# Kernel tuning notes

Hardware: AMD Instinct MI355X
Metric: run time of the kernel (lower is better)

The kernel has to match this reference:

```python
import jax, jax.numpy as jnp
import numpy as np

IN_F = 256
OUT_F = 256
HYPER = 128
BATCH = 4096


def setup_inputs() -> dict:
    key = jax.random.key(0)
    ks = jax.random.split(key, 9)
    s_in = 1.0 / np.sqrt(IN_F)
    s_h = 1.0 / np.sqrt(HYPER)
    x = jax.random.normal(ks[0], (BATCH, IN_F), dtype=jnp.float32)
    # weight_gen: Linear(in, hyper) -> ReLU -> Linear(hyper, in*out)
    W1g = jax.random.uniform(ks[1], (IN_F, HYPER), jnp.float32, -s_in, s_in)
    b1g = jax.random.uniform(ks[2], (HYPER,), jnp.float32, -s_in, s_in)
    W2g = jax.random.uniform(ks[3], (HYPER, IN_F * OUT_F), jnp.float32, -s_h, s_h)
    b2g = jax.random.uniform(ks[4], (IN_F * OUT_F,), jnp.float32, -s_h, s_h)
    # bias_gen: Linear(in, hyper) -> ReLU -> Linear(hyper, out)
    W1b = jax.random.uniform(ks[5], (IN_F, HYPER), jnp.float32, -s_in, s_in)
    b1b = jax.random.uniform(ks[6], (HYPER,), jnp.float32, -s_in, s_in)
    W2b = jax.random.uniform(ks[7], (HYPER, OUT_F), jnp.float32, -s_h, s_h)
    b2b = jax.random.uniform(ks[8], (OUT_F,), jnp.float32, -s_h, s_h)
    return {"x": x, "W1g": W1g, "b1g": b1g, "W2g": W2g, "b2g": b2g,
            "W1b": W1b, "b1b": b1b, "W2b": W2b, "b2b": b2b}


def reference(x, W1g, b1g, W2g, b2g, W1b, b1b, W2b, b2b):
    B = x.shape[0]
    # generate per-sample weights [B, out, in]
    hg = jax.nn.relu(x @ W1g + b1g)                      # [B, hyper]
    weights = (hg @ W2g + b2g).reshape(B, OUT_F, IN_F)   # [B, out, in]
    # generate per-sample bias [B, out]
    hb = jax.nn.relu(x @ W1b + b1b)                      # [B, hyper]
    bias = hb @ W2b + b2b                                # [B, out]
    # batched matvec: bmm(weights, x[...,None]) + bias
    out = jnp.einsum('boi,bi->bo', weights, x) + bias    # [B, out]
    return out
```

## Files before the change

kernel.cpp:

```cpp
#include <hip/hip_runtime.h>

#define AS1 __attribute__((address_space(1)))
#define AS3 __attribute__((address_space(3)))

typedef short short8 __attribute__((ext_vector_type(8)));
typedef float f32x16 __attribute__((ext_vector_type(16)));
typedef unsigned short ushort4v __attribute__((ext_vector_type(4)));

#define BATCH 4096
#define IN_F 256
#define OUT_F 256
#define HYP 128
#define HX 129
#define KP (HX * IN_F)
#define NGEMMP 32
#define NVB 516

__device__ __forceinline__ float bf2f(unsigned short u) {
  unsigned v = ((unsigned)u) << 16;
  float f;
  __builtin_memcpy(&f, &v, 4);
  return f;
}
__device__ __forceinline__ unsigned short f2bf(float f) {
  unsigned u;
  __builtin_memcpy(&u, &f, 4);
  unsigned r = u + 0x7fffu + ((u >> 16) & 1u);
  return (unsigned short)(r >> 16);
}

__device__ __forceinline__ void gld_lds16(const unsigned short* g, unsigned short* s) {
  __builtin_amdgcn_global_load_lds((const AS1 unsigned int*)g, (AS3 unsigned int*)s, 16, 0, 0);
}

__global__ __launch_bounds__(256) void k_trans(const float* __restrict__ W1g,
                                               const float* __restrict__ W1b,
                                               const float* __restrict__ W2b,
                                               unsigned short* __restrict__ W1T,
                                               unsigned short* __restrict__ W2bT) {
  const int t = threadIdx.x, b = blockIdx.x;
  if (b < 64) {
#pragma unroll
    for (int i = 0; i < 4; ++i) {
      const int e = b * 1024 + i * 256 + t;
      const int n = e >> 8, k = e & 255;
      const float v = (n < HYP) ? W1g[k * HYP + n] : W1b[k * HYP + (n - HYP)];
      W1T[e] = f2bf(v);
    }
  } else {
#pragma unroll
    for (int i = 0; i < 4; ++i) {
      const int e = (b - 64) * 1024 + i * 256 + t;
      const int o = e >> 7, h = e & 127;
      W2bT[e] = f2bf(W2b[h * OUT_F + o]);
    }
  }
}

__global__ __launch_bounds__(512) void k_prep(
    const float* __restrict__ x,
    const float* __restrict__ b1g, const float* __restrict__ b1b,
    const float* __restrict__ b2b,
    const float* __restrict__ W2g, const float* __restrict__ b2g,
    const unsigned short* __restrict__ W1T, const unsigned short* __restrict__ W2bT,
    unsigned short* __restrict__ Vb, unsigned short* __restrict__ hgbT,
    unsigned short* __restrict__ xb, float* __restrict__ out) {
  __shared__ __align__(16) unsigned short xS[128 * 256];
  __shared__ __align__(16) unsigned short hbS[128 * 128];
  const int t = threadIdx.x;

  if (blockIdx.x >= NGEMMP) {
    const int base = (blockIdx.x - NGEMMP) * 2048 + t;
#pragma unroll
    for (int it = 0; it < 4; ++it) {
      const int cid = base + it * 512;
      const int ic = cid & 31;
      const int pair = cid >> 5;
      const int h = pair % HX;
      const int o = pair / HX;
      const float* src = (h < HYP) ? (W2g + (size_t)h * (OUT_F * IN_F) + o * IN_F + ic * 8)
                                   : (b2g + o * IN_F + ic * 8);
      const float4 v0 = ((const float4*)src)[0];
      const float4 v1 = ((const float4*)src)[1];
      uint4 pk;
      pk.x = (unsigned)f2bf(v0.x) | ((unsigned)f2bf(v0.y) << 16);
      pk.y = (unsigned)f2bf(v0.z) | ((unsigned)f2bf(v0.w) << 16);
      pk.z = (unsigned)f2bf(v1.x) | ((unsigned)f2bf(v1.y) << 16);
      pk.w = (unsigned)f2bf(v1.z) | ((unsigned)f2bf(v1.w) << 16);
      *(uint4*)(Vb + (size_t)o * KP + h * IN_F + ic * 8) = pk;
    }
    return;
  }

  const int lane = t & 63;
  const int w = t >> 6;
  const int l31 = lane & 31;
  const int hi = lane >> 5;
  const int m0 = blockIdx.x * 128;

#pragma unroll
  for (int j = 0; j < 16; ++j) {
    const int row = j * 8 + w;
    const float4 v = *(const float4*)(x + (size_t)(m0 + row) * IN_F + lane * 4);
    uint2 pk;
    pk.x = (unsigned)f2bf(v.x) | ((unsigned)f2bf(v.y) << 16);
    pk.y = (unsigned)f2bf(v.z) | ((unsigned)f2bf(v.w) << 16);
    *(uint2*)(xb + (size_t)(m0 + row) * IN_F + lane * 4) = pk;
    const int ch = lane >> 1, half = lane & 1;
    *(uint2*)(&xS[row * 256 + ((ch ^ (row & 31))) * 8 + half * 4]) = pk;
  }
  __syncthreads();

  const int hA = w * 32 + l31;
  uint4 af[16];
#pragma unroll
  for (int kt = 0; kt < 16; ++kt)
    af[kt] = *(const uint4*)(W1T + (size_t)hA * 256 + kt * 16 + hi * 8);

  f32x16 zv;
#pragma unroll
  for (int i = 0; i < 16; ++i) zv[i] = 0.0f;
  f32x16 d0 = zv, d1 = zv, d2 = zv, d3 = zv;
#pragma unroll
  for (int kt = 0; kt < 16; ++kt) {
    const int pos = (kt * 2 + hi) ^ l31;
    const short8 a = __builtin_bit_cast(short8, af[kt]);
#define G1STEP(CS, DD)                                                        \
    {                                                                         \
      const short8 bfrg = *(const short8*)(&xS[(CS * 32 + l31) * 256 + pos * 8]); \
      DD = __builtin_amdgcn_mfma_f32_32x32x16_bf16(a, bfrg, DD, 0, 0, 0);     \
    }
    G1STEP(0, d0) G1STEP(1, d1) G1STEP(2, d2) G1STEP(3, d3)
#undef G1STEP
  }

  if (w < 4) {
    float4 bq[4];
#pragma unroll
    for (int q = 0; q < 4; ++q)
      bq[q] = *(const float4*)(b1g + w * 32 + q * 8 + hi * 4);
#define EPI_G(CS, DD)                                                         \
    {                                                                         \
      const int mcol = m0 + CS * 32 + l31;                                    \
      _Pragma("unroll")                                                       \
      for (int g = 0; g < 16; ++g) {                                          \
        const int h = w * 32 + (g & 3) + 8 * (g >> 2) + 4 * hi;               \
        float v = DD[g] + ((const float*)&bq[g >> 2])[g & 3];                 \
        v = v > 0.f ? v : 0.f;                                                \
        hgbT[(size_t)h * BATCH + mcol] = f2bf(v);                             \
      }                                                                       \
    }
    EPI_G(0, d0) EPI_G(1, d1) EPI_G(2, d2) EPI_G(3, d3)
#undef EPI_G
  } else {
    float4 bq[4];
#pragma unroll
    for (int q = 0; q < 4; ++q)
      bq[q] = *(const float4*)(b1b + (w - 4) * 32 + q * 8 + hi * 4);
#define EPI_B(CS, DD)                                                         \
    {                                                                         \
      const int m = CS * 32 + l31;                                            \
      _Pragma("unroll")                                                       \
      for (int q = 0; q < 4; ++q) {                                           \
        float v0 = DD[q * 4 + 0] + ((const float*)&bq[q])[0];                 \
        float v1 = DD[q * 4 + 1] + ((const float*)&bq[q])[1];                 \
        float v2 = DD[q * 4 + 2] + ((const float*)&bq[q])[2];                 \
        float v3 = DD[q * 4 + 3] + ((const float*)&bq[q])[3];                 \
        v0 = v0 > 0.f ? v0 : 0.f; v1 = v1 > 0.f ? v1 : 0.f;                   \
        v2 = v2 > 0.f ? v2 : 0.f; v3 = v3 > 0.f ? v3 : 0.f;                   \
        uint2 pk;                                                             \
        pk.x = (unsigned)f2bf(v0) | ((unsigned)f2bf(v1) << 16);               \
        pk.y = (unsigned)f2bf(v2) | ((unsigned)f2bf(v3) << 16);               \
        const int chunk = (w - 4) * 4 + q;                                    \
        *(uint2*)(&hbS[m * 128 + ((chunk ^ (m & 15))) * 8 + hi * 4]) = pk;    \
      }                                                                       \
    }
    EPI_B(0, d0) EPI_B(1, d1) EPI_B(2, d2) EPI_B(3, d3)
#undef EPI_B
  }
  __syncthreads();

  const int msub = w & 3, oh = w >> 2;
  const int mA = msub * 32 + l31;
  f32x16 e0 = zv, e1 = zv, e2 = zv, e3 = zv;
#pragma unroll
  for (int kt = 0; kt < 8; ++kt) {
    const int pos = (kt * 2 + hi) ^ (mA & 15);
    const short8 a = *(const short8*)(&hbS[mA * 128 + pos * 8]);
#define G2STEP(OS, EE)                                                        \
    {                                                                         \
      const int orow = oh * 128 + OS * 32 + l31;                              \
      const short8 bb = *(const short8*)(W2bT + (size_t)orow * 128 + kt * 16 + hi * 8); \
      EE = __builtin_amdgcn_mfma_f32_32x32x16_bf16(a, bb, EE, 0, 0, 0);       \
    }
    G2STEP(0, e0) G2STEP(1, e1) G2STEP(2, e2) G2STEP(3, e3)
#undef G2STEP
  }
#define EPI2(OS, EE)                                                          \
  {                                                                           \
    const int o = oh * 128 + OS * 32 + l31;                                   \
    const float bo = b2b[o];                                                  \
    _Pragma("unroll")                                                         \
    for (int g = 0; g < 16; ++g) {                                            \
      const int m = m0 + msub * 32 + (g & 3) + 8 * (g >> 2) + 4 * hi;         \
      out[(size_t)m * OUT_F + o] = EE[g] + bo;                                \
    }                                                                         \
  }
  EPI2(0, e0) EPI2(1, e1) EPI2(2, e2) EPI2(3, e3)
#undef EPI2
}

__global__ __launch_bounds__(256, 2)
void k_gemm(const unsigned short* __restrict__ Vb,
            const unsigned short* __restrict__ hgbT,
            const unsigned short* __restrict__ xb,
            float* __restrict__ out) {
  __shared__ __align__(16) unsigned short Bl[2][64 * 256];
  __shared__ __align__(16) unsigned short hgs[33 * 128];
  const int tid = threadIdx.x;
  const int lane = tid & 63;
  const int wave = tid >> 6;
  const int l31 = lane & 31;
  const int hi = lane >> 5;
  const int wm = wave & 1;
  const int wo = wave >> 1;

  const int bid = blockIdx.x;
  const int c = bid & 7;
  const int t2 = bid >> 3;
  const int xm = t2 & 31;
  const int g8 = t2 >> 5;
  const int grp = c + 8 * g8;
  const int yo = grp & 3;
  const int z = grp >> 2;

  const int m0 = xm * 128;
  const int o0 = yo * 64;
  const int hBeg = (z * HX) >> 2;
  const int hEnd = ((z + 1) * HX) >> 2;
  const int nh = hEnd - hBeg;

  for (int idx = tid; idx < nh * 128; idx += 256) {
    const int hl = idx >> 7;
    const int hh = hBeg + hl;
    hgs[idx] = (hh == HYP) ? (unsigned short)0x3F80
                           : hgbT[(size_t)hh * BATCH + m0 + (idx & 127)];
  }

  const int mrow0 = m0 + wm * 64 + l31;
  const int mrow1 = mrow0 + 32;
  uint4 xf0[16], xf1[16];
#pragma unroll
  for (int j = 0; j < 16; ++j) {
    xf0[j] = *(const uint4*)(xb + (size_t)mrow0 * IN_F + j * 16 + hi * 8);
    xf1[j] = *(const uint4*)(xb + (size_t)mrow1 * IN_F + j * 16 + hi * 8);
  }

  const int nB = tid >> 5;
  const int p5 = tid & 31;
  const int cs = p5 ^ (nB & 7);
  const unsigned short* gsrc = Vb + (size_t)(o0 + nB) * KP + cs * 8 + (size_t)hBeg * IN_F;

  f32x16 zv;
#pragma unroll
  for (int i = 0; i < 16; ++i) zv[i] = 0.0f;
  f32x16 acc0 = zv, acc1 = zv;
  f32x16 ah0 = zv, ah1 = zv;

#pragma unroll
  for (int j = 0; j < 8; ++j)
    gld_lds16(gsrc + (size_t)j * 8 * KP, &Bl[0][((size_t)tid + 256 * j) * 8]);
  __syncthreads();

  const int rowb = wo * 32 + l31;
  for (int r = 0; r < nh; ++r) {
    const int buf = r & 1;
    if (r + 1 < nh) {
      const unsigned short* gs = gsrc + (size_t)(r + 1) * IN_F;
#pragma unroll
      for (int j = 0; j < 8; ++j)
        gld_lds16(gs + (size_t)j * 8 * KP, &Bl[buf ^ 1][((size_t)tid + 256 * j) * 8]);
    }
    const unsigned short* bp = &Bl[buf][0];
#pragma unroll
    for (int ic = 0; ic < 4; ++ic) {
#pragma unroll
      for (int t = 0; t < 4; ++t) {
        const int c0 = ic * 8 + t * 2 + hi;
        const int pr = c0 ^ (l31 & 7);
        const short8 b0 = *(const short8*)(bp + rowb * 256 + pr * 8);
        const short8 a0 = __builtin_bit_cast(short8, xf0[ic * 4 + t]);
        const short8 a1 = __builtin_bit_cast(short8, xf1[ic * 4 + t]);
        if (ic == 0 && t == 0) {
          ah0 = __builtin_amdgcn_mfma_f32_32x32x16_bf16(a0, b0, zv, 0, 0, 0);
          ah1 = __builtin_amdgcn_mfma_f32_32x32x16_bf16(a1, b0, zv, 0, 0, 0);
        } else {
          ah0 = __builtin_amdgcn_mfma_f32_32x32x16_bf16(a0, b0, ah0, 0, 0, 0);
          ah1 = __builtin_amdgcn_mfma_f32_32x32x16_bf16(a1, b0, ah1, 0, 0, 0);
        }
      }
    }
#pragma unroll
    for (int q = 0; q < 4; ++q) {
      const ushort4v v0 = *(const ushort4v*)&hgs[r * 128 + wm * 64 + 4 * hi + q * 8];
      const ushort4v v1 = *(const ushort4v*)&hgs[r * 128 + wm * 64 + 32 + 4 * hi + q * 8];
#pragma unroll
      for (int e = 0; e < 4; ++e) {
        acc0[q * 4 + e] += bf2f(v0[e]) * ah0[q * 4 + e];
        acc1[q * 4 + e] += bf2f(v1[e]) * ah1[q * 4 + e];
      }
    }
    __syncthreads();
  }

  const int mb = m0 + wm * 64 + 4 * hi;
  const int col = o0 + wo * 32 + l31;
#pragma unroll
  for (int g = 0; g < 16; ++g) {
    const int row0 = mb + (g & 3) + 8 * (g >> 2);
    atomicAdd(&out[(size_t)row0 * OUT_F + col], acc0[g]);
    atomicAdd(&out[(size_t)(row0 + 32) * OUT_F + col], acc1[g]);
  }
}

extern "C" void kernel_launch(void* const* d_in, const int* in_sizes, int n_in,
                              void* d_out, int out_size, void* d_ws, size_t ws_size,
                              hipStream_t stream) {
  const float* x = (const float*)d_in[0];
  const float* W1g = (const float*)d_in[1];
  const float* b1g = (const float*)d_in[2];
  const float* W2g = (const float*)d_in[3];
  const float* b2g = (const float*)d_in[4];
  const float* W1b = (const float*)d_in[5];
  const float* b1b = (const float*)d_in[6];
  const float* W2b = (const float*)d_in[7];
  const float* b2b = (const float*)d_in[8];
  float* out = (float*)d_out;

  char* ws = (char*)d_ws;
  const size_t szV = (size_t)OUT_F * KP * 2;
  const size_t szHg = (size_t)HYP * BATCH * 2;
  const size_t szXb = (size_t)BATCH * IN_F * 2;
  const size_t szW1T = (size_t)256 * 256 * 2;
  unsigned short* Vb = (unsigned short*)ws;
  unsigned short* hgbT = (unsigned short*)(ws + szV);
  unsigned short* xb = (unsigned short*)(ws + szV + szHg);
  unsigned short* W1T = (unsigned short*)(ws + szV + szHg + szXb);
  unsigned short* W2bT = (unsigned short*)(ws + szV + szHg + szXb + szW1T);

  hipLaunchKernelGGL(k_trans, dim3(96), dim3(256), 0, stream, W1g, W1b, W2b, W1T, W2bT);
  hipLaunchKernelGGL(k_prep, dim3(NGEMMP + NVB), dim3(512), 0, stream,
                     x, b1g, b1b, b2b, W2g, b2g, W1T, W2bT, Vb, hgbT, xb, out);
  hipLaunchKernelGGL(k_gemm, dim3(512), dim3(256), 0, stream, Vb, hgbT, xb, out);
}
```

Before: 187.9 us.

## Shrink k_gemm tile to 32 outputs per block with 8-way hyper split

Reshapes the main GEMM tiling so each block covers 128 batch rows by 32 output columns instead of 64. The hyper dimension is split 8 ways instead of 4, and each wave now computes a single 32x32 MFMA tile. LDS per block shrinks, launch bounds allow 4 blocks per CU, and the grid grows from 512 to 2048 blocks to raise occupancy and latency hiding. In exchange, each B fragment from LDS now feeds one MFMA instead of two, x fragments are reloaded by more blocks, and the number of float atomicAdds into the output doubles.

Result: slower. 194.5 us (+3.5%).

```diff
diff --git a/kernel.cpp b/kernel.cpp
--- a/kernel.cpp
+++ b/kernel.cpp
@@ -210,20 +210,18 @@
 #undef EPI2
 }
 
-__global__ __launch_bounds__(256, 2)
+__global__ __launch_bounds__(256, 4)
 void k_gemm(const unsigned short* __restrict__ Vb,
             const unsigned short* __restrict__ hgbT,
             const unsigned short* __restrict__ xb,
             float* __restrict__ out) {
-  __shared__ __align__(16) unsigned short Bl[2][64 * 256];
-  __shared__ __align__(16) unsigned short hgs[33 * 128];
+  __shared__ __align__(16) unsigned short Bl[2][32 * 256];
+  __shared__ __align__(16) unsigned short hgs[17 * 128];
   const int tid = threadIdx.x;
   const int lane = tid & 63;
   const int wave = tid >> 6;
   const int l31 = lane & 31;
   const int hi = lane >> 5;
-  const int wm = wave & 1;
-  const int wo = wave >> 1;
 
   const int bid = blockIdx.x;
   const int c = bid & 7;
@@ -231,13 +229,13 @@
   const int xm = t2 & 31;
   const int g8 = t2 >> 5;
   const int grp = c + 8 * g8;
-  const int yo = grp & 3;
-  const int z = grp >> 2;
+  const int yo = grp & 7;
+  const int z = grp >> 3;
 
   const int m0 = xm * 128;
-  const int o0 = yo * 64;
-  const int hBeg = (z * HX) >> 2;
-  const int hEnd = ((z + 1) * HX) >> 2;
+  const int o0 = yo * 32;
+  const int hBeg = (z * HX) >> 3;
+  const int hEnd = ((z + 1) * HX) >> 3;
   const int nh = hEnd - hBeg;
 
   for (int idx = tid; idx < nh * 128; idx += 256) {
@@ -247,14 +245,11 @@
                            : hgbT[(size_t)hh * BATCH + m0 + (idx & 127)];
   }
 
-  const int mrow0 = m0 + wm * 64 + l31;
-  const int mrow1 = mrow0 + 32;
-  uint4 xf0[16], xf1[16];
-#pragma unroll
-  for (int j = 0; j < 16; ++j) {
-    xf0[j] = *(const uint4*)(xb + (size_t)mrow0 * IN_F + j * 16 + hi * 8);
-    xf1[j] = *(const uint4*)(xb + (size_t)mrow1 * IN_F + j * 16 + hi * 8);
-  }
+  const int mrow = m0 + wave * 32 + l31;
+  uint4 xf[16];
+#pragma unroll
+  for (int j = 0; j < 16; ++j)
+    xf[j] = *(const uint4*)(xb + (size_t)mrow * IN_F + j * 16 + hi * 8);
 
   const int nB = tid >> 5;
   const int p5 = tid & 31;
@@ -264,62 +259,49 @@
   f32x16 zv;
 #pragma unroll
   for (int i = 0; i < 16; ++i) zv[i] = 0.0f;
-  f32x16 acc0 = zv, acc1 = zv;
-  f32x16 ah0 = zv, ah1 = zv;
-
-#pragma unroll
-  for (int j = 0; j < 8; ++j)
+  f32x16 acc = zv, ah = zv;
+
+#pragma unroll
+  for (int j = 0; j < 4; ++j)
     gld_lds16(gsrc + (size_t)j * 8 * KP, &Bl[0][((size_t)tid + 256 * j) * 8]);
   __syncthreads();
 
-  const int rowb = wo * 32 + l31;
   for (int r = 0; r < nh; ++r) {
     const int buf = r & 1;
     if (r + 1 < nh) {
       const unsigned short* gs = gsrc + (size_t)(r + 1) * IN_F;
 #pragma unroll
-      for (int j = 0; j < 8; ++j)
+      for (int j = 0; j < 4; ++j)
         gld_lds16(gs + (size_t)j * 8 * KP, &Bl[buf ^ 1][((size_t)tid + 256 * j) * 8]);
     }
     const unsigned short* bp = &Bl[buf][0];
 #pragma unroll
-    for (int ic = 0; ic < 4; ++ic) {
-#pragma unroll
-      for (int t = 0; t < 4; ++t) {
-        const int c0 = ic * 8 + t * 2 + hi;
-        const int pr = c0 ^ (l31 & 7);
-        const short8 b0 = *(const short8*)(bp + rowb * 256 + pr * 8);
-        const short8 a0 = __builtin_bit_cast(short8, xf0[ic * 4 + t]);
-        const short8 a1 = __builtin_bit_cast(short8, xf1[ic * 4 + t]);
-        if (ic == 0 && t == 0) {
-          ah0 = __builtin_amdgcn_mfma_f32_32x32x16_bf16(a0, b0, zv, 0, 0, 0);
-          ah1 = __builtin_amdgcn_mfma_f32_32x32x16_bf16(a1, b0, zv, 0, 0, 0);
-        } else {
-          ah0 = __builtin_amdgcn_mfma_f32_32x32x16_bf16(a0, b0, ah0, 0, 0, 0);
-          ah1 = __builtin_amdgcn_mfma_f32_32x32x16_bf16(a1, b0, ah1, 0, 0, 0);
-        }
-      }
+    for (int kt = 0; kt < 16; ++kt) {
+      const int c0 = kt * 2 + hi;
+      const int pr = c0 ^ (l31 & 7);
+      const short8 b0 = *(const short8*)(bp + l31 * 256 + pr * 8);
+      const short8 a0 = __builtin_bit_cast(short8, xf[kt]);
+      if (kt == 0)
+        ah = __builtin_amdgcn_mfma_f32_32x32x16_bf16(a0, b0, zv, 0, 0, 0);
+      else
+        ah = __builtin_amdgcn_mfma_f32_32x32x16_bf16(a0, b0, ah, 0, 0, 0);
     }
 #pragma unroll
     for (int q = 0; q < 4; ++q) {
-      const ushort4v v0 = *(const ushort4v*)&hgs[r * 128 + wm * 64 + 4 * hi + q * 8];
-      const ushort4v v1 = *(const ushort4v*)&hgs[r * 128 + wm * 64 + 32 + 4 * hi + q * 8];
-#pragma unroll
-      for (int e = 0; e < 4; ++e) {
-        acc0[q * 4 + e] += bf2f(v0[e]) * ah0[q * 4 + e];
-        acc1[q * 4 + e] += bf2f(v1[e]) * ah1[q * 4 + e];
-      }
+      const ushort4v v0 = *(const ushort4v*)&hgs[r * 128 + wave * 32 + 4 * hi + q * 8];
+#pragma unroll
+      for (int e = 0; e < 4; ++e)
+        acc[q * 4 + e] += bf2f(v0[e]) * ah[q * 4 + e];
     }
     __syncthreads();
   }
 
-  const int mb = m0 + wm * 64 + 4 * hi;
-  const int col = o0 + wo * 32 + l31;
+  const int mb = m0 + wave * 32 + 4 * hi;
+  const int col = o0 + l31;
 #pragma unroll
   for (int g = 0; g < 16; ++g) {
     const int row0 = mb + (g & 3) + 8 * (g >> 2);
-    atomicAdd(&out[(size_t)row0 * OUT_F + col], acc0[g]);
-    atomicAdd(&out[(size_t)(row0 + 32) * OUT_F + col], acc1[g]);
+    atomicAdd(&out[(size_t)row0 * OUT_F + col], acc[g]);
   }
 }
 
@@ -351,5 +333,5 @@
   hipLaunchKernelGGL(k_trans, dim3(96), dim3(256), 0, stream, W1g, W1b, W2b, W1T, W2bT);
   hipLaunchKernelGGL(k_prep, dim3(NGEMMP + NVB), dim3(512), 0, stream,
                      x, b1g, b1b, b2b, W2g, b2g, W1T, W2bT, Vb, hgbT, xb, out);
-  hipLaunchKernelGGL(k_gemm, dim3(512), dim3(256), 0, stream, Vb, hgbT, xb, out);
-}
+  hipLaunchKernelGGL(k_gemm, dim3(2048), dim3(256), 0, stream, Vb, hgbT, xb, out);
+}
```

## Load B operand directly into registers with double-buffered prefetch instead of LDS

Applied to the files above, without the earlier changes.

Replaces the LDS staging of the generated-weight tile (global_load_lds into a double-buffered shared array, plus a block barrier per hyper row) with direct global loads of each wave's B fragments into two register buffers. The loop is unrolled by two so one buffer is consumed while the other is filled. This removes the per-iteration __syncthreads and the LDS round trip. In exchange it uses far more VGPRs, so launch bounds drop to one block per CU. Each wave now loads its own B rows, so the two waves sharing the same wo both fetch the same data from global/L2 instead of sharing one LDS copy.

After: 247.0 us. +31.5%, slower.

```diff
diff --git a/kernel.cpp b/kernel.cpp
--- a/kernel.cpp
+++ b/kernel.cpp
@@ -27,10 +27,6 @@
   __builtin_memcpy(&u, &f, 4);
   unsigned r = u + 0x7fffu + ((u >> 16) & 1u);
   return (unsigned short)(r >> 16);
-}
-
-__device__ __forceinline__ void gld_lds16(const unsigned short* g, unsigned short* s) {
-  __builtin_amdgcn_global_load_lds((const AS1 unsigned int*)g, (AS3 unsigned int*)s, 16, 0, 0);
 }
 
 __global__ __launch_bounds__(256) void k_trans(const float* __restrict__ W1g,
@@ -210,12 +206,11 @@
 #undef EPI2
 }
 
-__global__ __launch_bounds__(256, 2)
+__global__ __launch_bounds__(256, 1)
 void k_gemm(const unsigned short* __restrict__ Vb,
             const unsigned short* __restrict__ hgbT,
             const unsigned short* __restrict__ xb,
             float* __restrict__ out) {
-  __shared__ __align__(16) unsigned short Bl[2][64 * 256];
   __shared__ __align__(16) unsigned short hgs[33 * 128];
   const int tid = threadIdx.x;
   const int lane = tid & 63;
@@ -256,62 +251,68 @@
     xf1[j] = *(const uint4*)(xb + (size_t)mrow1 * IN_F + j * 16 + hi * 8);
   }
 
-  const int nB = tid >> 5;
-  const int p5 = tid & 31;
-  const int cs = p5 ^ (nB & 7);
-  const unsigned short* gsrc = Vb + (size_t)(o0 + nB) * KP + cs * 8 + (size_t)hBeg * IN_F;
+  const unsigned short* bbase =
+      Vb + (size_t)(o0 + wo * 32 + l31) * KP + (size_t)hBeg * IN_F + hi * 8;
 
   f32x16 zv;
 #pragma unroll
   for (int i = 0; i < 16; ++i) zv[i] = 0.0f;
   f32x16 acc0 = zv, acc1 = zv;
-  f32x16 ah0 = zv, ah1 = zv;
-
-#pragma unroll
-  for (int j = 0; j < 8; ++j)
-    gld_lds16(gsrc + (size_t)j * 8 * KP, &Bl[0][((size_t)tid + 256 * j) * 8]);
+
+  uint4 bufA[16], bufB[16];
+#pragma unroll
+  for (int j = 0; j < 16; ++j)
+    bufA[j] = *(const uint4*)(bbase + j * 16);
+
   __syncthreads();
 
-  const int rowb = wo * 32 + l31;
-  for (int r = 0; r < nh; ++r) {
-    const int buf = r & 1;
+#define COMPUTE(BUF, RR)                                                      \
+  {                                                                           \
+    f32x16 ah0, ah1;                                                          \
+    _Pragma("unroll")                                                         \
+    for (int j = 0; j < 16; ++j) {                                            \
+      const short8 b0 = __builtin_bit_cast(short8, BUF[j]);                   \
+      const short8 a0 = __builtin_bit_cast(short8, xf0[j]);                   \
+      const short8 a1 = __builtin_bit_cast(short8, xf1[j]);                   \
+      if (j == 0) {                                                           \
+        ah0 = __builtin_amdgcn_mfma_f32_32x32x16_bf16(a0, b0, zv, 0, 0, 0);   \
+        ah1 = __builtin_amdgcn_mfma_f32_32x32x16_bf16(a1, b0, zv, 0, 0, 0);   \
+      } else {                                                                \
+        ah0 = __builtin_amdgcn_mfma_f32_32x32x16_bf16(a0, b0, ah0, 0, 0, 0);  \
+        ah1 = __builtin_amdgcn_mfma_f32_32x32x16_bf16(a1, b0, ah1, 0, 0, 0);  \
+      }                                                                       \
+    }                                                                         \
+    _Pragma("unroll")                                                         \
+    for (int q = 0; q < 4; ++q) {                                             \
+      const ushort4v v0 = *(const ushort4v*)&hgs[(RR) * 128 + wm * 64 + 4 * hi + q * 8]; \
+      const ushort4v v1 = *(const ushort4v*)&hgs[(RR) * 128 + wm * 64 + 32 + 4 * hi + q * 8]; \
+      _Pragma("unroll")                                                       \
+      for (int e = 0; e < 4; ++e) {                                           \
+        acc0[q * 4 + e] += bf2f(v0[e]) * ah0[q * 4 + e];                      \
+        acc1[q * 4 + e] += bf2f(v1[e]) * ah1[q * 4 + e];                      \
+      }                                                                       \
+    }                                                                         \
+  }
+
+  for (int r = 0; r < nh; r += 2) {
     if (r + 1 < nh) {
-      const unsigned short* gs = gsrc + (size_t)(r + 1) * IN_F;
-#pragma unroll
-      for (int j = 0; j < 8; ++j)
-        gld_lds16(gs + (size_t)j * 8 * KP, &Bl[buf ^ 1][((size_t)tid + 256 * j) * 8]);
-    }
-    const unsigned short* bp = &Bl[buf][0];
-#pragma unroll
-    for (int ic = 0; ic < 4; ++ic) {
-#pragma unroll
-      for (int t = 0; t < 4; ++t) {
-        const int c0 = ic * 8 + t * 2 + hi;
-        const int pr = c0 ^ (l31 & 7);
-        const short8 b0 = *(const short8*)(bp + rowb * 256 + pr * 8);
-        const short8 a0 = __builtin_bit_cast(short8, xf0[ic * 4 + t]);
-        const short8 a1 = __builtin_bit_cast(short8, xf1[ic * 4 + t]);
-        if (ic == 0 && t == 0) {
-          ah0 = __builtin_amdgcn_mfma_f32_32x32x16_bf16(a0, b0, zv, 0, 0, 0);
-          ah1 = __builtin_amdgcn_mfma_f32_32x32x16_bf16(a1, b0, zv, 0, 0, 0);
-        } else {
-          ah0 = __builtin_amdgcn_mfma_f32_32x32x16_bf16(a0, b0, ah0, 0, 0, 0);
-          ah1 = __builtin_amdgcn_mfma_f32_32x32x16_bf16(a1, b0, ah1, 0, 0, 0);
-        }
+      const unsigned short* bp = bbase + (size_t)(r + 1) * IN_F;
+#pragma unroll
+      for (int j = 0; j < 16; ++j)
+        bufB[j] = *(const uint4*)(bp + j * 16);
+    }
+    COMPUTE(bufA, r)
+    if (r + 1 < nh) {
+      if (r + 2 < nh) {
+        const unsigned short* bp = bbase + (size_t)(r + 2) * IN_F;
+#pragma unroll
+        for (int j = 0; j < 16; ++j)
+          bufA[j] = *(const uint4*)(bp + j * 16);
       }
-    }
-#pragma unroll
-    for (int q = 0; q < 4; ++q) {
-      const ushort4v v0 = *(const ushort4v*)&hgs[r * 128 + wm * 64 + 4 * hi + q * 8];
-      const ushort4v v1 = *(const ushort4v*)&hgs[r * 128 + wm * 64 + 32 + 4 * hi + q * 8];
-#pragma unroll
-      for (int e = 0; e < 4; ++e) {
-        acc0[q * 4 + e] += bf2f(v0[e]) * ah0[q * 4 + e];
-        acc1[q * 4 + e] += bf2f(v1[e]) * ah1[q * 4 + e];
-      }
-    }
-    __syncthreads();
-  }
+      COMPUTE(bufB, r + 1)
+    }
+  }
+#undef COMPUTE
 
   const int mb = m0 + wm * 64 + 4 * hi;
   const int col = o0 + wo * 32 + l31;
```
